# Optimization experiments

Hardware: AMD Instinct MI355X
Metric: run time of the kernel (lower is better)

## Reference

```python
import jax, jax.numpy as jnp
import numpy as np
from jax.ops import segment_sum

N_NODES = 100000
N_EDGES = 1600000
N_GRAPHS = 128


def setup_inputs() -> dict:
    key = jax.random.key(0)
    ks = jax.random.split(key, 16)
    x = jax.random.normal(ks[0], (N_NODES, 128), dtype=jnp.float32)
    edge_index = jax.random.randint(ks[1], (2, N_EDGES), 0, N_NODES, dtype=jnp.int64)
    batch = jnp.sort(jax.random.randint(ks[2], (N_NODES,), 0, N_GRAPHS, dtype=jnp.int64))
    def glorot(k, fan_in, fan_out):
        lim = (6.0 / (fan_in + fan_out)) ** 0.5
        return jax.random.uniform(k, (fan_in, fan_out), jnp.float32, -lim, lim)
    return {
        "x": x, "edge_index": edge_index, "batch": batch,
        "W1": glorot(ks[3], 128, 64), "b1": jnp.zeros((64,), jnp.float32),
        "W2": glorot(ks[4], 64, 64),  "b2": jnp.zeros((64,), jnp.float32),
        "W3": glorot(ks[5], 64, 64),  "b3": jnp.zeros((64,), jnp.float32),
        "W4": glorot(ks[6], 64, 64),  "b4": jnp.zeros((64,), jnp.float32),
        "Wl": glorot(ks[7], 64, 1),   "bl": jnp.zeros((1,), jnp.float32),
    }


def _gcn_layer(x, row, col, norm, W, b):
    # x: [N, Cin] -> [N, Cout]; gather source feats, scale, scatter-add at target
    h = x @ W                                 # dense transform first (GCNConv order)
    msg = norm[:, None] * h[row]              # [E, Cout]
    out = segment_sum(msg, col, num_segments=N_NODES)
    return out + b


def reference(x, edge_index, batch, W1, b1, W2, b2, W3, b3, W4, b4, Wl, bl):
    row, col = edge_index[0], edge_index[1]
    # symmetric degree normalization based on in-degree of col (PyG degree(col))
    deg = segment_sum(jnp.ones((N_EDGES,), x.dtype), col, num_segments=N_NODES)
    dinv = jnp.where(deg > 0, deg ** -0.5, jnp.zeros_like(deg))
    norm = dinv[row] * dinv[col]              # [E]

    h = _gcn_layer(x, row, col, norm, W1, b1)
    h = _gcn_layer(h, row, col, norm, W2, b2)
    h = _gcn_layer(h, row, col, norm, W3, b3)
    h = _gcn_layer(h, row, col, norm, W4, b4)  # [N, 64]

    # to_dense_batch + mean(dim=1): padded zeros count, so divide by max graph size
    sums = segment_sum(h, batch, num_segments=N_GRAPHS)          # [B, 64]
    counts = segment_sum(jnp.ones((N_NODES,), h.dtype), batch, num_segments=N_GRAPHS)
    n_max = jnp.max(counts)
    pooled = sums / n_max                                        # [B, 64]
    return pooled @ Wl + bl                                      # [B, 1]
```

## Files before the change

kernel.cpp:

```cpp
#include <hip/hip_runtime.h>
#include <hip/hip_bf16.h>
#include <hip/hip_fp16.h>

#define N_NODES 100000
#define N_EDGES 1600000
#define N_GRAPHS 128

#define BSH 9
#define BNODES 512
#define NB 196
#define CAP 12288
#define BLK 512
#define EPB (N_EDGES / BLK)
#define RECMAX 10240

#define SPLIT 4


__global__ __launch_bounds__(256) void k_hist(const int* __restrict__ col,
                                              int* __restrict__ hist_t) {
    __shared__ int h[NB];
    const int t = threadIdx.x, b = blockIdx.x;
    for (int i = t; i < NB; i += 256) h[i] = 0;
    __syncthreads();
    const int e0 = b * EPB;
    for (int i = t; i < EPB; i += 256) atomicAdd(&h[col[e0 + i] >> BSH], 1);
    __syncthreads();
    for (int i = t; i < NB; i += 256) hist_t[i * BLK + b] = h[i];
}

__global__ __launch_bounds__(512) void k_cursors(const int* __restrict__ hist_t,
                                                 int* __restrict__ cursors,
                                                 int* __restrict__ bcnt) {
    __shared__ int s[BLK];
    const int t = threadIdx.x, bin = blockIdx.x;
    const int v = hist_t[bin * BLK + t];
    s[t] = v; __syncthreads();
    for (int off = 1; off < BLK; off <<= 1) {
        int a = (t >= off) ? s[t - off] : 0;
        __syncthreads(); s[t] += a; __syncthreads();
    }
    cursors[bin * BLK + t] = bin * CAP + s[t] - v;
    if (t == BLK - 1) bcnt[bin] = s[t];
}

__global__ __launch_bounds__(256) void k_mid(const int* __restrict__ row,
                                             const int* __restrict__ col,
                                             const int* __restrict__ cursors,
                                             int* __restrict__ bedges) {
    __shared__ int cur[NB];
    const int t = threadIdx.x, b = blockIdx.x;
    for (int i = t; i < NB; i += 256) cur[i] = cursors[i * BLK + b];
    __syncthreads();
    const int e0 = b * EPB;
    for (int i = t; i < EPB; i += 256) {
        const int c = col[e0 + i];
        const int r = row[e0 + i];
        const int pos = atomicAdd(&cur[c >> BSH], 1);
        bedges[pos] = r | ((c & (BNODES - 1)) << 17);
    }
}

__global__ __launch_bounds__(512) void k_build(const int* __restrict__ bedges,
                                               const int* __restrict__ bcnt,
                                               int* __restrict__ csr,
                                               int* __restrict__ offs,
                                               int* __restrict__ deg_c,
                                               float* __restrict__ dinv) {
    __shared__ int rec[RECMAX];
    __shared__ int deg[BNODES];
    __shared__ int offx[BNODES];
    __shared__ int cur[BNODES];
    const int t = threadIdx.x, bin = blockIdx.x;
    const int base = bin * CAP;
    const int cnt = bcnt[bin];
    const int vb = bin << BSH;
    const int nn = min(BNODES, N_NODES - vb);
    for (int i = t; i < cnt; i += 512) rec[i] = bedges[base + i];
    deg[t] = 0;
    __syncthreads();
    for (int i = t; i < cnt; i += 512) atomicAdd(&deg[(rec[i] >> 17) & (BNODES - 1)], 1);
    __syncthreads();
    const int d = (t < nn) ? deg[t] : 0;
    const int pd = (d + 7) & ~7;
    offx[t] = pd; __syncthreads();
    for (int off = 1; off < BNODES; off <<= 1) {
        int a = (t >= off) ? offx[t - off] : 0;
        __syncthreads(); offx[t] += a; __syncthreads();
    }
    const int myoff = offx[t] - pd;
    cur[t] = myoff;
    if (t < nn) {
        offs[vb + t] = base + myoff;
        deg_c[vb + t] = d;
        dinv[vb + t] = (d > 0) ? rsqrtf((float)d) : 0.0f;
        for (int j = d; j < pd; j++) csr[base + myoff + j] = N_NODES;
    }
    __syncthreads();
    for (int i = t; i < cnt; i += 512) {
        const int r = rec[i];
        const int pos = atomicAdd(&cur[(r >> 17) & (BNODES - 1)], 1);
        csr[base + pos] = r & 0x1FFFF;
    }
}


template <int CIN>
__global__ __launch_bounds__(256) void k_gemm(const float* __restrict__ X,
                                              const float* __restrict__ W,
                                              const float* __restrict__ dinv,
                                              __half* __restrict__ H16) {
    constexpr int STR = 66;
    __shared__ float sX[128 * STR];
    __shared__ float sW[64 * 64];
    const int t = threadIdx.x;
    const int nb = blockIdx.x * 128;
    const int tx = t & 7;
    const int ty = t >> 3;
    const int c0 = tx * 8, n0 = ty * 4;

    float acc[4][8] = {};

    for (int k0 = 0; k0 < CIN; k0 += 64) {
        if (k0) __syncthreads();
        for (int i = t; i < 64 * 16; i += 256) {
            const int k = i >> 4, c4 = (i & 15) * 4;
            *reinterpret_cast<float4*>(&sW[k * 64 + c4]) =
                *reinterpret_cast<const float4*>(W + (size_t)(k0 + k) * 64 + c4);
        }
        for (int i = t; i < 128 * 16; i += 256) {
            const int node = i >> 4, k4 = (i & 15) * 4;
            const int gn = nb + node;
            float4 v = make_float4(0.f, 0.f, 0.f, 0.f);
            if (gn < N_NODES)
                v = *reinterpret_cast<const float4*>(X + (size_t)gn * CIN + k0 + k4);
            float* dst = &sX[node * STR + k4];
            *reinterpret_cast<float2*>(dst) = make_float2(v.x, v.y);
            *reinterpret_cast<float2*>(dst + 2) = make_float2(v.z, v.w);
        }
        __syncthreads();

        const float* xb = &sX[n0 * STR];
        #pragma unroll 4
        for (int k = 0; k < 64; k++) {
            const float4 b0 = *reinterpret_cast<const float4*>(&sW[k * 64 + c0]);
            const float4 b1 = *reinterpret_cast<const float4*>(&sW[k * 64 + c0 + 4]);
            const float a0 = xb[k];
            const float a1 = xb[STR + k];
            const float a2 = xb[2 * STR + k];
            const float a3 = xb[3 * STR + k];
            acc[0][0] += a0 * b0.x; acc[0][1] += a0 * b0.y; acc[0][2] += a0 * b0.z; acc[0][3] += a0 * b0.w;
            acc[0][4] += a0 * b1.x; acc[0][5] += a0 * b1.y; acc[0][6] += a0 * b1.z; acc[0][7] += a0 * b1.w;
            acc[1][0] += a1 * b0.x; acc[1][1] += a1 * b0.y; acc[1][2] += a1 * b0.z; acc[1][3] += a1 * b0.w;
            acc[1][4] += a1 * b1.x; acc[1][5] += a1 * b1.y; acc[1][6] += a1 * b1.z; acc[1][7] += a1 * b1.w;
            acc[2][0] += a2 * b0.x; acc[2][1] += a2 * b0.y; acc[2][2] += a2 * b0.z; acc[2][3] += a2 * b0.w;
            acc[2][4] += a2 * b1.x; acc[2][5] += a2 * b1.y; acc[2][6] += a2 * b1.z; acc[2][7] += a2 * b1.w;
            acc[3][0] += a3 * b0.x; acc[3][1] += a3 * b0.y; acc[3][2] += a3 * b0.z; acc[3][3] += a3 * b0.w;
            acc[3][4] += a3 * b1.x; acc[3][5] += a3 * b1.y; acc[3][6] += a3 * b1.z; acc[3][7] += a3 * b1.w;
        }
    }

    #pragma unroll
    for (int n = 0; n < 4; n++) {
        const int gn = nb + n0 + n;
        if (gn < N_NODES) {
            const float dv = dinv[gn];
            __half2 h[4];
            #pragma unroll
            for (int q = 0; q < 4; q++)
                h[q] = __floats2half2_rn(acc[n][2 * q] * dv, acc[n][2 * q + 1] * dv);
            *reinterpret_cast<int4*>(H16 + (size_t)gn * 64 + c0) =
                *reinterpret_cast<const int4*>(h);
        }
    }
}


__global__ __launch_bounds__(256) void k_prop(const __half* __restrict__ Hin,
                                              const int* __restrict__ csr,
                                              const int* __restrict__ offs,
                                              const int* __restrict__ deg_c,
                                              const float* __restrict__ dinv,
                                              const float* __restrict__ bias,
                                              float* __restrict__ Hout) {
    const int wave = threadIdx.x >> 6, lane = threadIdx.x & 63;
    const int half = lane >> 5;
    const int c2 = lane & 31;
    const int v = (blockIdx.x * 4 + wave) * 2 + half;
    const int start = offs[v];
    const int cntp = (deg_c[v] + 7) & ~7;
    const int* ep = csr + start;
    const __half* hb = Hin + c2 * 2;
    float ax = 0.f, ay = 0.f;
    for (int j = 0; j < cntp; j += 8) {
        const int4 q0 = *reinterpret_cast<const int4*>(ep + j);
        const int4 q1 = *reinterpret_cast<const int4*>(ep + j + 4);
        const float2 f0 = __half22float2(*reinterpret_cast<const __half2*>(hb + (size_t)q0.x * 64));
        const float2 f1 = __half22float2(*reinterpret_cast<const __half2*>(hb + (size_t)q0.y * 64));
        const float2 f2 = __half22float2(*reinterpret_cast<const __half2*>(hb + (size_t)q0.z * 64));
        const float2 f3 = __half22float2(*reinterpret_cast<const __half2*>(hb + (size_t)q0.w * 64));
        const float2 f4 = __half22float2(*reinterpret_cast<const __half2*>(hb + (size_t)q1.x * 64));
        const float2 f5 = __half22float2(*reinterpret_cast<const __half2*>(hb + (size_t)q1.y * 64));
        const float2 f6 = __half22float2(*reinterpret_cast<const __half2*>(hb + (size_t)q1.z * 64));
        const float2 f7 = __half22float2(*reinterpret_cast<const __half2*>(hb + (size_t)q1.w * 64));
        ax += ((f0.x + f1.x) + (f2.x + f3.x)) + ((f4.x + f5.x) + (f6.x + f7.x));
        ay += ((f0.y + f1.y) + (f2.y + f3.y)) + ((f4.y + f5.y) + (f6.y + f7.y));
    }
    const float dv = dinv[v];
    float2 o;
    o.x = dv * ax + bias[c2 * 2];
    o.y = dv * ay + bias[c2 * 2 + 1];
    *reinterpret_cast<float2*>(Hout + (size_t)v * 64 + c2 * 2) = o;
}


__global__ __launch_bounds__(256) void k_pool(const float* __restrict__ H,
                                              const int* __restrict__ batch,
                                              float* __restrict__ partial) {
    const int g = blockIdx.x >> 2;
    const int s = blockIdx.x & (SPLIT - 1);
    int lo = 0, hi = N_NODES;
    while (lo < hi) { int m = (lo + hi) >> 1; if (batch[m] < g) lo = m + 1; else hi = m; }
    const int a = lo;
    lo = 0; hi = N_NODES;
    while (lo < hi) { int m = (lo + hi) >> 1; if (batch[m] < g + 1) lo = m + 1; else hi = m; }
    const int b = lo;

    const int wave = threadIdx.x >> 6, lane = threadIdx.x & 63;
    const int lane16 = s * 4 + wave;
    float ac0 = 0.f, ac1 = 0.f, ac2 = 0.f, ac3 = 0.f;
    int v = a + lane16;
    for (; v + 48 < b; v += 64) {
        ac0 += H[(size_t)v * 64 + lane];
        ac1 += H[(size_t)(v + 16) * 64 + lane];
        ac2 += H[(size_t)(v + 32) * 64 + lane];
        ac3 += H[(size_t)(v + 48) * 64 + lane];
    }
    for (; v < b; v += 16) ac0 += H[(size_t)v * 64 + lane];
    const float acc = (ac0 + ac1) + (ac2 + ac3);

    __shared__ float red[4][64];
    red[wave][lane] = acc;
    __syncthreads();
    if (wave == 0) {
        const float r = (red[0][lane] + red[1][lane]) + (red[2][lane] + red[3][lane]);
        partial[((size_t)s * N_GRAPHS + g) * 64 + lane] = r;
    }
}

__global__ void k_final(const float* __restrict__ partial, const int* __restrict__ batch,
                        const float* __restrict__ Wl, const float* __restrict__ bl,
                        float* __restrict__ out) {
    __shared__ int scnt[128];
    int t = threadIdx.x;
    int lo = 0, hi = N_NODES;
    while (lo < hi) { int mid = (lo + hi) >> 1; if (batch[mid] < t) lo = mid + 1; else hi = mid; }
    int a = lo;
    lo = 0; hi = N_NODES;
    while (lo < hi) { int mid = (lo + hi) >> 1; if (batch[mid] < t + 1) lo = mid + 1; else hi = mid; }
    scnt[t] = lo - a;
    __syncthreads();
    for (int off = 64; off > 0; off >>= 1) {
        if (t < off) scnt[t] = max(scnt[t], scnt[t + off]);
        __syncthreads();
    }
    const float nmax = (float)scnt[0];
    float s = 0.f;
    for (int c = 0; c < 64; c++) {
        float g = 0.f;
        #pragma unroll
        for (int p = 0; p < SPLIT; p++)
            g += partial[((size_t)p * N_GRAPHS + t) * 64 + c];
        s += g * Wl[c];
    }
    out[t] = s / nmax + bl[0];
}


extern "C" void kernel_launch(void* const* d_in, const int* in_sizes, int n_in,
                              void* d_out, int out_size, void* d_ws, size_t ws_size,
                              hipStream_t stream) {
    const float* x    = (const float*)d_in[0];
    const int*   ei   = (const int*)d_in[1];
    const int*   batch= (const int*)d_in[2];
    const float* W1 = (const float*)d_in[3];  const float* b1 = (const float*)d_in[4];
    const float* W2 = (const float*)d_in[5];  const float* b2 = (const float*)d_in[6];
    const float* W3 = (const float*)d_in[7];  const float* b3 = (const float*)d_in[8];
    const float* W4 = (const float*)d_in[9];  const float* b4 = (const float*)d_in[10];
    const float* Wl = (const float*)d_in[11]; const float* bl = (const float*)d_in[12];
    float* out = (float*)d_out;

    const int* row = ei;
    const int* col = ei + N_EDGES;

    char* ws = (char*)d_ws;
    size_t off = 0;
    auto alloc = [&](size_t bytes) {
        void* p = ws + off;
        off = (off + bytes + 255) & ~(size_t)255;
        return p;
    };
    int*    hist_t  = (int*)alloc((size_t)NB * BLK * 4);
    int*    cursors = (int*)alloc((size_t)NB * BLK * 4);
    int*    bcnt    = (int*)alloc(NB * 4);
    int*    bedges  = (int*)alloc((size_t)NB * CAP * 4);
    int*    csr     = bedges;
    int*    offs    = (int*)alloc(N_NODES * 4);
    int*    deg_c   = (int*)alloc(N_NODES * 4);
    float*  dinv    = (float*)alloc(N_NODES * 4);
    __half* h16     = (__half*)alloc((size_t)(N_NODES + 1) * 64 * 2);
    float*  h_b     = (float*)alloc((size_t)N_NODES * 64 * 4);
    float*  partial = (float*)alloc((size_t)SPLIT * N_GRAPHS * 64 * 4);

    hipMemsetAsync(h16 + (size_t)N_NODES * 64, 0, 64 * 2, stream);

    k_hist<<<BLK, 256, 0, stream>>>(col, hist_t);
    k_cursors<<<NB, 512, 0, stream>>>(hist_t, cursors, bcnt);
    k_mid<<<BLK, 256, 0, stream>>>(row, col, cursors, bedges);
    k_build<<<NB, 512, 0, stream>>>(bedges, bcnt, csr, offs, deg_c, dinv);

    const int GB = (N_NODES + 127) / 128;
    const int PB = N_NODES / 8;

    k_gemm<128><<<GB, 256, 0, stream>>>(x, W1, dinv, h16);
    k_prop<<<PB, 256, 0, stream>>>(h16, csr, offs, deg_c, dinv, b1, h_b);
    k_gemm<64><<<GB, 256, 0, stream>>>(h_b, W2, dinv, h16);
    k_prop<<<PB, 256, 0, stream>>>(h16, csr, offs, deg_c, dinv, b2, h_b);
    k_gemm<64><<<GB, 256, 0, stream>>>(h_b, W3, dinv, h16);
    k_prop<<<PB, 256, 0, stream>>>(h16, csr, offs, deg_c, dinv, b3, h_b);
    k_gemm<64><<<GB, 256, 0, stream>>>(h_b, W4, dinv, h16);
    k_prop<<<PB, 256, 0, stream>>>(h16, csr, offs, deg_c, dinv, b4, h_b);

    k_pool<<<N_GRAPHS * SPLIT, 256, 0, stream>>>(h_b, batch, partial);
    k_final<<<1, 128, 0, stream>>>(partial, batch, Wl, bl, out);
}
```

Measured before the change: 407.2 us.

## Use f16 MFMA with split-precision weights for GCN dense transform

Replaces the scalar FP32 register-tiled GEMM in k_gemm with MFMA 16x16x32 f16 instructions. Activations are converted to f16, and weights are split into hi and lo f16 parts so that two MFMAs per tile recover most of the weight precision. The aim is to cut the ALU time of the transform stage. In exchange, activation precision drops to f16 and the output stores become scattered 2-byte writes instead of 16-byte vector stores.

```diff
diff --git a/kernel.cpp b/kernel.cpp
--- a/kernel.cpp
+++ b/kernel.cpp
@@ -15,6 +15,9 @@
 #define RECMAX 10240
 
 #define SPLIT 4
+
+typedef __attribute__((ext_vector_type(8))) _Float16 v8h;
+typedef __attribute__((ext_vector_type(4))) float v4f;
 
 
 __global__ __launch_bounds__(256) void k_hist(const int* __restrict__ col,
@@ -110,23 +113,30 @@
                                               const float* __restrict__ W,
                                               const float* __restrict__ dinv,
                                               __half* __restrict__ H16) {
-    constexpr int STR = 66;
-    __shared__ float sX[128 * STR];
-    __shared__ float sW[64 * 64];
+    constexpr int SA = 72;
+    constexpr int SB = 72;
+    __shared__ __align__(16) _Float16 sA[128 * SA];
+    __shared__ __align__(16) _Float16 sBh[64 * SB];
+    __shared__ __align__(16) _Float16 sBl[64 * SB];
     const int t = threadIdx.x;
+    const int w = t >> 6, lane = t & 63;
+    const int quad = lane >> 4, l16 = lane & 15;
     const int nb = blockIdx.x * 128;
-    const int tx = t & 7;
-    const int ty = t >> 3;
-    const int c0 = tx * 8, n0 = ty * 4;
-
-    float acc[4][8] = {};
+
+    v4f acc[2][4] = {};
 
     for (int k0 = 0; k0 < CIN; k0 += 64) {
         if (k0) __syncthreads();
         for (int i = t; i < 64 * 16; i += 256) {
             const int k = i >> 4, c4 = (i & 15) * 4;
-            *reinterpret_cast<float4*>(&sW[k * 64 + c4]) =
-                *reinterpret_cast<const float4*>(W + (size_t)(k0 + k) * 64 + c4);
+            const float4 wv = *reinterpret_cast<const float4*>(W + (size_t)(k0 + k) * 64 + c4);
+            const float wf[4] = {wv.x, wv.y, wv.z, wv.w};
+            #pragma unroll
+            for (int j = 0; j < 4; j++) {
+                const _Float16 hi = (_Float16)wf[j];
+                sBh[(c4 + j) * SB + k] = hi;
+                sBl[(c4 + j) * SB + k] = (_Float16)(wf[j] - (float)hi);
+            }
         }
         for (int i = t; i < 128 * 16; i += 256) {
             const int node = i >> 4, k4 = (i & 15) * 4;
@@ -134,43 +144,46 @@
             float4 v = make_float4(0.f, 0.f, 0.f, 0.f);
             if (gn < N_NODES)
                 v = *reinterpret_cast<const float4*>(X + (size_t)gn * CIN + k0 + k4);
-            float* dst = &sX[node * STR + k4];
-            *reinterpret_cast<float2*>(dst) = make_float2(v.x, v.y);
-            *reinterpret_cast<float2*>(dst + 2) = make_float2(v.z, v.w);
+            _Float16* d = &sA[node * SA + k4];
+            d[0] = (_Float16)v.x; d[1] = (_Float16)v.y;
+            d[2] = (_Float16)v.z; d[3] = (_Float16)v.w;
         }
         __syncthreads();
 
-        const float* xb = &sX[n0 * STR];
-        #pragma unroll 4
-        for (int k = 0; k < 64; k++) {
-            const float4 b0 = *reinterpret_cast<const float4*>(&sW[k * 64 + c0]);
-            const float4 b1 = *reinterpret_cast<const float4*>(&sW[k * 64 + c0 + 4]);
-            const float a0 = xb[k];
-            const float a1 = xb[STR + k];
-            const float a2 = xb[2 * STR + k];
-            const float a3 = xb[3 * STR + k];
-            acc[0][0] += a0 * b0.x; acc[0][1] += a0 * b0.y; acc[0][2] += a0 * b0.z; acc[0][3] += a0 * b0.w;
-            acc[0][4] += a0 * b1.x; acc[0][5] += a0 * b1.y; acc[0][6] += a0 * b1.z; acc[0][7] += a0 * b1.w;
-            acc[1][0] += a1 * b0.x; acc[1][1] += a1 * b0.y; acc[1][2] += a1 * b0.z; acc[1][3] += a1 * b0.w;
-            acc[1][4] += a1 * b1.x; acc[1][5] += a1 * b1.y; acc[1][6] += a1 * b1.z; acc[1][7] += a1 * b1.w;
-            acc[2][0] += a2 * b0.x; acc[2][1] += a2 * b0.y; acc[2][2] += a2 * b0.z; acc[2][3] += a2 * b0.w;
-            acc[2][4] += a2 * b1.x; acc[2][5] += a2 * b1.y; acc[2][6] += a2 * b1.z; acc[2][7] += a2 * b1.w;
-            acc[3][0] += a3 * b0.x; acc[3][1] += a3 * b0.y; acc[3][2] += a3 * b0.z; acc[3][3] += a3 * b0.w;
-            acc[3][4] += a3 * b1.x; acc[3][5] += a3 * b1.y; acc[3][6] += a3 * b1.z; acc[3][7] += a3 * b1.w;
+        #pragma unroll
+        for (int kt = 0; kt < 2; kt++) {
+            const int kb = kt * 32 + quad * 8;
+            v8h afr[2], bh[4], bl[4];
+            #pragma unroll
+            for (int mt = 0; mt < 2; mt++)
+                afr[mt] = *reinterpret_cast<const v8h*>(&sA[(w * 32 + mt * 16 + l16) * SA + kb]);
+            #pragma unroll
+            for (int nt = 0; nt < 4; nt++) {
+                bh[nt] = *reinterpret_cast<const v8h*>(&sBh[(nt * 16 + l16) * SB + kb]);
+                bl[nt] = *reinterpret_cast<const v8h*>(&sBl[(nt * 16 + l16) * SB + kb]);
+            }
+            #pragma unroll
+            for (int mt = 0; mt < 2; mt++)
+                #pragma unroll
+                for (int nt = 0; nt < 4; nt++) {
+                    acc[mt][nt] = __builtin_amdgcn_mfma_f32_16x16x32_f16(afr[mt], bh[nt], acc[mt][nt], 0, 0, 0);
+                    acc[mt][nt] = __builtin_amdgcn_mfma_f32_16x16x32_f16(afr[mt], bl[nt], acc[mt][nt], 0, 0, 0);
+                }
         }
     }
 
     #pragma unroll
-    for (int n = 0; n < 4; n++) {
-        const int gn = nb + n0 + n;
-        if (gn < N_NODES) {
-            const float dv = dinv[gn];
-            __half2 h[4];
-            #pragma unroll
-            for (int q = 0; q < 4; q++)
-                h[q] = __floats2half2_rn(acc[n][2 * q] * dv, acc[n][2 * q + 1] * dv);
-            *reinterpret_cast<int4*>(H16 + (size_t)gn * 64 + c0) =
-                *reinterpret_cast<const int4*>(h);
+    for (int mt = 0; mt < 2; mt++) {
+        #pragma unroll
+        for (int reg = 0; reg < 4; reg++) {
+            const int node = nb + w * 32 + mt * 16 + quad * 4 + reg;
+            if (node < N_NODES) {
+                const float dv = dinv[node];
+                #pragma unroll
+                for (int nt = 0; nt < 4; nt++)
+                    H16[(size_t)node * 64 + nt * 16 + l16] =
+                        __float2half(acc[mt][nt][reg] * dv);
+            }
         }
     }
 }
```

Result: faster. 367.3 us (-9.8%).
